# Optimization experiments

Hardware: AMD Instinct MI355X
Metric: run time of the kernel (lower is better)

Reference implementation:

```python
import jax, jax.numpy as jnp
import numpy as np

N_NODES = 100000
N_EDGES = 3200000
IN_CH = 24
HIDDEN = 64
N_CLASSES = 16


def _sage_conv(x, src, dst, W_l, b_l, W_r, num_nodes):
    # mean-aggregate neighbor features at destination nodes
    msg = x[src]                                             # [E, F] gather
    agg = jax.ops.segment_sum(msg, dst, num_segments=num_nodes)
    deg = jax.ops.segment_sum(jnp.ones((src.shape[0],), x.dtype), dst,
                              num_segments=num_nodes)
    mean = agg / jnp.maximum(deg, 1.0)[:, None]
    # PyG SAGEConv: lin_l(aggregated) + lin_r(self); bias lives in lin_l
    return mean @ W_l.T + b_l + x @ W_r.T


def setup_inputs() -> dict:
    key = jax.random.key(0)
    ks = jax.random.split(key, 8)
    x = jax.random.normal(ks[0], (N_NODES, IN_CH), dtype=jnp.float32)
    edge_index = jax.random.randint(ks[1], (2, N_EDGES), 0, N_NODES, dtype=jnp.int64)
    s1 = 1.0 / np.sqrt(IN_CH)
    s2 = 1.0 / np.sqrt(HIDDEN)
    return {
        "x": x,
        "edge_index": edge_index,
        "W1_l": jax.random.normal(ks[2], (HIDDEN, IN_CH), dtype=jnp.float32) * s1,
        "b1": jnp.zeros((HIDDEN,), jnp.float32),
        "W1_r": jax.random.normal(ks[3], (HIDDEN, IN_CH), dtype=jnp.float32) * s1,
        "W2_l": jax.random.normal(ks[4], (HIDDEN, HIDDEN), dtype=jnp.float32) * s2,
        "b2": jnp.zeros((HIDDEN,), jnp.float32),
        "W2_r": jax.random.normal(ks[5], (HIDDEN, HIDDEN), dtype=jnp.float32) * s2,
        "Wc": jax.random.normal(ks[6], (N_CLASSES, HIDDEN), dtype=jnp.float32) * s2,
        "bc": jnp.zeros((N_CLASSES,), jnp.float32),
    }


def reference(x, edge_index, W1_l, b1, W1_r, W2_l, b2, W2_r, Wc, bc):
    num_nodes = x.shape[0]
    src, dst = edge_index[0], edge_index[1]
    h = _sage_conv(x, src, dst, W1_l, b1, W1_r, num_nodes)
    h = jax.nn.relu(h)
    # dropout is identity in eval mode
    embeddings = _sage_conv(h, src, dst, W2_l, b2, W2_r, num_nodes)
    logits = embeddings @ Wc.T + bc
    return (logits, embeddings)
```

## Files before the change

kernel.cpp:

```cpp
#include <hip/hip_runtime.h>

#define N_NODES 100000
#define N_EDGES 3200000
#define IN_CH 24
#define HIDDEN 64
#define N_CLASSES 16

#define NBUCK 782
#define PHBLOCKS 512
#define PHCHUNK 6250
#define PTBLOCKS 256
#define PTCHUNK 12500
#define NSTRIPS (N_NODES / 16)

typedef __attribute__((ext_vector_type(8))) short short8;
typedef __attribute__((ext_vector_type(4))) float float4_;
typedef __attribute__((ext_vector_type(2))) float float2v;

__device__ __forceinline__ unsigned short f2bf(float f) {
    union { float f; unsigned int u; } v; v.f = f;
    unsigned int u = v.u;
    return (unsigned short)((u + 0x7FFFu + ((u >> 16) & 1u)) >> 16);
}
__device__ __forceinline__ unsigned short pk_fp8(float a, float b) {
    return (unsigned short)(__builtin_amdgcn_cvt_pk_fp8_f32(a, b, 0, false) & 0xFFFF);
}
__device__ __forceinline__ void accum8(float2v* A, uint2 u) {
    A[0] += __builtin_amdgcn_cvt_pk_f32_fp8(u.x, false);
    A[1] += __builtin_amdgcn_cvt_pk_f32_fp8(u.x, true);
    A[2] += __builtin_amdgcn_cvt_pk_f32_fp8(u.y, false);
    A[3] += __builtin_amdgcn_cvt_pk_f32_fp8(u.y, true);
}


__global__ __launch_bounds__(1024) void k_phist(const int* __restrict__ dst,
                                                int* __restrict__ bucketCnt) {
    __shared__ int hist[NBUCK];
    int t = threadIdx.x;
    int cbeg = blockIdx.x * PHCHUNK;
    for (int i = t; i < NBUCK; i += 1024) hist[i] = 0;
    __syncthreads();
#pragma unroll
    for (int k = 0; k < 7; k++) {
        int o = k * 1024 + t;
        if (o < PHCHUNK) atomicAdd(&hist[dst[cbeg + o] >> 7], 1);
    }
    __syncthreads();
    for (int i = t; i < NBUCK; i += 1024)
        if (hist[i]) atomicAdd(&bucketCnt[i], hist[i]);
}

__global__ __launch_bounds__(1024) void k_scanb(const int* __restrict__ bucketCnt,
                                                int* __restrict__ bucketBase,
                                                int* __restrict__ bucketFill,
                                                int* __restrict__ srcs, int E) {
    __shared__ int lds[1024];
    int t = threadIdx.x;
    int c = (t < NBUCK) ? bucketCnt[t] : 0;
    int val = c;
    lds[t] = val;
    __syncthreads();
    for (int off = 1; off < 1024; off <<= 1) {
        int v = (t >= off) ? lds[t - off] : 0;
        __syncthreads();
        val += v;
        lds[t] = val;
        __syncthreads();
    }
    if (t < NBUCK) {
        int ex = val - c;
        bucketBase[t] = ex;
        bucketFill[t] = ex;
    }
    if (t == 0) bucketBase[NBUCK] = E;
    if (t < 32) srcs[E + t] = 0;
}

__global__ __launch_bounds__(1024) void k_part(const int* __restrict__ src,
                                               const int* __restrict__ dst,
                                               int* __restrict__ bucketFill,
                                               unsigned int* __restrict__ pedges) {
    __shared__ int cntL[NBUCK];
    __shared__ int baseL[NBUCK];
    int t = threadIdx.x;
    int cbeg = blockIdx.x * PTCHUNK;
    int d[13], s[13];
#pragma unroll
    for (int k = 0; k < 13; k++) {
        int o = k * 1024 + t;
        bool ok = o < PTCHUNK;
        d[k] = ok ? dst[cbeg + o] : -1;
        s[k] = ok ? src[cbeg + o] : 0;
    }
    for (int i = t; i < NBUCK; i += 1024) cntL[i] = 0;
    __syncthreads();
#pragma unroll
    for (int k = 0; k < 13; k++)
        if (d[k] >= 0) atomicAdd(&cntL[d[k] >> 7], 1);
    __syncthreads();
    for (int i = t; i < NBUCK; i += 1024) {
        int c = cntL[i];
        if (c) baseL[i] = atomicAdd(&bucketFill[i], c);
        cntL[i] = 0;
    }
    __syncthreads();
#pragma unroll
    for (int k = 0; k < 13; k++)
        if (d[k] >= 0) {
            int bk = d[k] >> 7;
            int r = atomicAdd(&cntL[bk], 1);
            pedges[baseL[bk] + r] = ((unsigned int)(d[k] & 127) << 17) | (unsigned int)s[k];
        }
}

__global__ __launch_bounds__(1024) void k_bucket(const unsigned int* __restrict__ pedges,
                                                 const int* __restrict__ bucketBase,
                                                 int* __restrict__ rowptr,
                                                 int* __restrict__ srcs, int N, int E) {
    __shared__ int ncnt[128];
    __shared__ int sps[128];
    int b = blockIdx.x;
    int t = threadIdx.x;
    int eb = bucketBase[b], ee = bucketBase[b + 1];
    int m = ee - eb;
    unsigned int v[8];
#pragma unroll
    for (int k = 0; k < 8; k++) {
        int o = k * 1024 + t;
        v[k] = (o < m) ? pedges[eb + o] : 0xFFFFFFFFu;
    }
    if (t < 128) ncnt[t] = 0;
    __syncthreads();
#pragma unroll
    for (int k = 0; k < 8; k++)
        if (v[k] != 0xFFFFFFFFu) atomicAdd(&ncnt[v[k] >> 17], 1);
    __syncthreads();
    int myc = (t < 128) ? ncnt[t] : 0;
    int val = myc;
    if (t < 128) sps[t] = val;
    __syncthreads();
    for (int off = 1; off < 128; off <<= 1) {
        int vv = (t >= off && t < 128) ? sps[t - off] : 0;
        __syncthreads();
        if (t < 128) { val += vv; sps[t] = val; }
        __syncthreads();
    }
    int mybase = val - myc;
    int node = b * 128 + t;
    if (t < 128 && node < N) rowptr[node] = eb + mybase;
    if (b == 0 && t == 0) rowptr[N] = E;
    if (t < 128) { sps[t] = mybase; ncnt[t] = 0; }
    __syncthreads();
#pragma unroll
    for (int k = 0; k < 8; k++)
        if (v[k] != 0xFFFFFFFFu) {
            unsigned int nl = v[k] >> 17;
            int r = atomicAdd(&ncnt[nl], 1);
            srcs[eb + sps[nl] + r] = (int)(v[k] & 0x1FFFF);
        }
}


__global__ __launch_bounds__(256) void k_prep(const float* __restrict__ W1l,
                                              const float* __restrict__ W1r,
                                              const float* __restrict__ W2l,
                                              const float* __restrict__ W2r,
                                              const float* __restrict__ Wc,
                                              const float* __restrict__ b2,
                                              const float* __restrict__ bc,
                                              unsigned short* __restrict__ Bt1,
                                              unsigned short* __restrict__ Bt2,
                                              float* __restrict__ bias2) {
    int t = threadIdx.x;
    for (int i = t; i < 64 * 64; i += 256) {
        int o = i >> 6, k = i & 63;
        float v = (k < 24) ? W1r[o * 24 + k] : ((k < 48) ? W1l[o * 24 + k - 24] : 0.f);
        Bt1[i] = f2bf(v);
    }
    for (int i = t; i < 64 * 128; i += 256) {
        int o = i >> 7, k = i & 127;
        float v = (k < 64) ? W2l[o * 64 + k] : W2r[o * 64 + k - 64];
        Bt2[i] = f2bf(v);
    }
    for (int i = t; i < 16 * 128; i += 256) {
        int c = i >> 7, k = i & 127;
        const float* M = (k < 64) ? W2l : W2r;
        int kk = k & 63;
        float s = 0.f;
        for (int j = 0; j < 64; j++) s += Wc[c * 64 + j] * M[j * 64 + kk];
        Bt2[(64 + c) * 128 + k] = f2bf(s);
    }
    for (int i = t; i < 80; i += 256) {
        if (i < 64) bias2[i] = b2[i];
        else {
            int c = i - 64;
            float s = bc[c];
            for (int j = 0; j < 64; j++) s += Wc[c * 64 + j] * b2[j];
            bias2[i] = s;
        }
    }
}

__global__ __launch_bounds__(256) void k_castx(const float* __restrict__ x,
                                               unsigned int* __restrict__ A1u,
                                               unsigned short* __restrict__ X8s) {
    int gid = blockIdx.x * 256 + threadIdx.x;
    if (gid >= N_NODES * 16) return;
    int n = gid >> 4, kp = gid & 15;
    if (kp < 12) {
        const float2 v = *(const float2*)(x + n * 24 + kp * 2);
        A1u[n * 32 + kp] = (unsigned int)f2bf(v.x) | ((unsigned int)f2bf(v.y) << 16);
        X8s[n * 16 + kp] = pk_fp8(v.x, v.y);
    } else {
        int p = kp - 12;
        uint2 z; z.x = 0u; z.y = 0u;
        *(uint2*)(A1u + n * 32 + 24 + p * 2) = z;
        X8s[n * 16 + kp] = 0;
    }
}


__global__ __launch_bounds__(256) void k_agg1(const unsigned int* __restrict__ X8u,
                                              const int* __restrict__ rowptr,
                                              const int* __restrict__ srcs,
                                              unsigned int* __restrict__ A1w, int N) {
    int node = (blockIdx.x * 256 + threadIdx.x) >> 6;
    int lane = threadIdx.x & 63;
    if (node >= N) return;
    int b = rowptr[node], e = rowptr[node + 1];
    int grp = lane >> 2;
    int sub = lane & 3;
    const unsigned int* basep = X8u + sub * 2;
    float2v A[4] = {{0.f, 0.f}, {0.f, 0.f}, {0.f, 0.f}, {0.f, 0.f}};
    int nfull = (e - b) & ~31;
    int j = b;
    for (; j < b + nfull; j += 32) {
        int s0 = srcs[j + grp];
        int s1 = srcs[j + 16 + grp];
        uint2 u0 = *(const uint2*)(basep + (size_t)s0 * 8);
        uint2 u1 = *(const uint2*)(basep + (size_t)s1 * 8);
        accum8(A, u0);
        accum8(A, u1);
    }
    if (j < e) {
        int j0 = j + grp, j1 = j0 + 16;
        int s0 = srcs[j0], s1 = srcs[j1];
        uint2 u0 = *(const uint2*)(basep + (size_t)s0 * 8);
        uint2 u1 = *(const uint2*)(basep + (size_t)s1 * 8);
        if (j0 >= e) { u0.x = 0; u0.y = 0; }
        if (j1 >= e) { u1.x = 0; u1.y = 0; }
        accum8(A, u0);
        accum8(A, u1);
    }
#pragma unroll
    for (int m = 4; m <= 32; m <<= 1) {
#pragma unroll
        for (int q = 0; q < 4; q++) {
            A[q].x += __shfl_xor(A[q].x, m, 64);
            A[q].y += __shfl_xor(A[q].y, m, 64);
        }
    }
    if (lane < 4) {
        float inv = 1.f / (float)max(e - b, 1);
        uint4 o;
        o.x = (unsigned int)f2bf(A[0].x * inv) | ((unsigned int)f2bf(A[0].y * inv) << 16);
        o.y = (unsigned int)f2bf(A[1].x * inv) | ((unsigned int)f2bf(A[1].y * inv) << 16);
        o.z = (unsigned int)f2bf(A[2].x * inv) | ((unsigned int)f2bf(A[2].y * inv) << 16);
        o.w = (unsigned int)f2bf(A[3].x * inv) | ((unsigned int)f2bf(A[3].y * inv) << 16);
        *(uint4*)(A1w + (size_t)node * 32 + 12 + sub * 4) = o;
    }
}

__global__ __launch_bounds__(256) void k_agg2(const unsigned int* __restrict__ H8u,
                                              const int* __restrict__ rowptr,
                                              const int* __restrict__ srcs,
                                              unsigned int* __restrict__ A2w, int N) {
    int node = (blockIdx.x * 256 + threadIdx.x) >> 6;
    int lane = threadIdx.x & 63;
    if (node >= N) return;
    int b = rowptr[node], e = rowptr[node + 1];
    int grp = lane >> 3;
    int sub = lane & 7;
    const unsigned int* basep = H8u + sub * 2;
    float2v A[4] = {{0.f, 0.f}, {0.f, 0.f}, {0.f, 0.f}, {0.f, 0.f}};
    int nfull = (e - b) & ~31;
    int j = b;
    for (; j < b + nfull; j += 32) {
        int s0 = srcs[j + grp];
        int s1 = srcs[j + 8 + grp];
        int s2 = srcs[j + 16 + grp];
        int s3 = srcs[j + 24 + grp];
        uint2 u0 = *(const uint2*)(basep + (size_t)s0 * 16);
        uint2 u1 = *(const uint2*)(basep + (size_t)s1 * 16);
        uint2 u2 = *(const uint2*)(basep + (size_t)s2 * 16);
        uint2 u3 = *(const uint2*)(basep + (size_t)s3 * 16);
        accum8(A, u0);
        accum8(A, u1);
        accum8(A, u2);
        accum8(A, u3);
    }
    if (j < e) {
        int j0 = j + grp, j1 = j0 + 8, j2 = j0 + 16, j3 = j0 + 24;
        int s0 = srcs[j0], s1 = srcs[j1], s2 = srcs[j2], s3 = srcs[j3];
        uint2 u0 = *(const uint2*)(basep + (size_t)s0 * 16);
        uint2 u1 = *(const uint2*)(basep + (size_t)s1 * 16);
        uint2 u2 = *(const uint2*)(basep + (size_t)s2 * 16);
        uint2 u3 = *(const uint2*)(basep + (size_t)s3 * 16);
        if (j0 >= e) { u0.x = 0; u0.y = 0; }
        if (j1 >= e) { u1.x = 0; u1.y = 0; }
        if (j2 >= e) { u2.x = 0; u2.y = 0; }
        if (j3 >= e) { u3.x = 0; u3.y = 0; }
        accum8(A, u0);
        accum8(A, u1);
        accum8(A, u2);
        accum8(A, u3);
    }
#pragma unroll
    for (int m = 8; m <= 32; m <<= 1) {
#pragma unroll
        for (int q = 0; q < 4; q++) {
            A[q].x += __shfl_xor(A[q].x, m, 64);
            A[q].y += __shfl_xor(A[q].y, m, 64);
        }
    }
    if (lane < 8) {
        float inv = 1.f / (float)max(e - b, 1);
        uint4 o;
        o.x = (unsigned int)f2bf(A[0].x * inv) | ((unsigned int)f2bf(A[0].y * inv) << 16);
        o.y = (unsigned int)f2bf(A[1].x * inv) | ((unsigned int)f2bf(A[1].y * inv) << 16);
        o.z = (unsigned int)f2bf(A[2].x * inv) | ((unsigned int)f2bf(A[2].y * inv) << 16);
        o.w = (unsigned int)f2bf(A[3].x * inv) | ((unsigned int)f2bf(A[3].y * inv) << 16);
        *(uint4*)(A2w + (size_t)node * 64 + sub * 4) = o;
    }
}


__global__ __launch_bounds__(256) void k_gemm1(const unsigned short* __restrict__ A1,
                                               const unsigned short* __restrict__ Bt1,
                                               const float* __restrict__ b1,
                                               unsigned short* __restrict__ A2s,
                                               unsigned char* __restrict__ H8b) {
    int wave = (blockIdx.x * 256 + threadIdx.x) >> 6;
    int lane = threadIdx.x & 63;
    int m = lane & 15, quad = lane >> 4;
    if (wave >= NSTRIPS) return;
    short8 bf[4][2];
#pragma unroll
    for (int t = 0; t < 4; t++)
#pragma unroll
        for (int s = 0; s < 2; s++)
            bf[t][s] = *(const short8*)(Bt1 + (t * 16 + m) * 64 + s * 32 + quad * 8);
    float bias[4];
#pragma unroll
    for (int t = 0; t < 4; t++) bias[t] = b1[t * 16 + m];

    int row0 = wave * 16;
    short8 a0 = *(const short8*)(A1 + (row0 + m) * 64 + quad * 8);
    short8 a1 = *(const short8*)(A1 + (row0 + m) * 64 + 32 + quad * 8);
    float4_ acc[4];
#pragma unroll
    for (int t = 0; t < 4; t++) {
        float4_ c = {0.f, 0.f, 0.f, 0.f};
        c = __builtin_amdgcn_mfma_f32_16x16x32_bf16(a0, bf[t][0], c, 0, 0, 0);
        c = __builtin_amdgcn_mfma_f32_16x16x32_bf16(a1, bf[t][1], c, 0, 0, 0);
        acc[t] = c;
    }
#pragma unroll
    for (int t = 0; t < 4; t++) {
        int col = t * 16 + m;
#pragma unroll
        for (int r = 0; r < 4; r++) {
            int row = row0 + quad * 4 + r;
            float v = fmaxf(acc[t][r] + bias[t], 0.f);
            A2s[row * 128 + 64 + col] = f2bf(v);
            H8b[row * 64 + col] =
                (unsigned char)(__builtin_amdgcn_cvt_pk_fp8_f32(v, 0.f, 0, false) & 0xFF);
        }
    }
}

__global__ __launch_bounds__(256) void k_gemm2(const unsigned short* __restrict__ Bt2,
                                               const float* __restrict__ bias2,
                                               unsigned short* A2s,
                                               float* logits) {
    int wave = (blockIdx.x * 256 + threadIdx.x) >> 6;
    int lane = threadIdx.x & 63;
    int m = lane & 15, quad = lane >> 4;
    if (wave >= NSTRIPS) return;
    short8 bf[5][4];
#pragma unroll
    for (int t = 0; t < 5; t++)
#pragma unroll
        for (int s = 0; s < 4; s++)
            bf[t][s] = *(const short8*)(Bt2 + (t * 16 + m) * 128 + s * 32 + quad * 8);
    float bias[5];
#pragma unroll
    for (int t = 0; t < 5; t++) bias[t] = bias2[t * 16 + m];

    int row0 = wave * 16;
    short8 a[4];
#pragma unroll
    for (int s = 0; s < 4; s++)
        a[s] = *(const short8*)(A2s + (row0 + m) * 128 + s * 32 + quad * 8);
    float4_ acc[5];
#pragma unroll
    for (int t = 0; t < 5; t++) {
        float4_ c = {0.f, 0.f, 0.f, 0.f};
#pragma unroll
        for (int s = 0; s < 4; s++)
            c = __builtin_amdgcn_mfma_f32_16x16x32_bf16(a[s], bf[t][s], c, 0, 0, 0);
        acc[t] = c;
    }
    float* embp = (float*)A2s;
#pragma unroll
    for (int t = 0; t < 4; t++) {
#pragma unroll
        for (int r = 0; r < 4; r++) {
            int row = row0 + quad * 4 + r;
            embp[row * 64 + t * 16 + m] = acc[t][r] + bias[t];
        }
    }
#pragma unroll
    for (int r = 0; r < 4; r++) {
        int row = row0 + quad * 4 + r;
        logits[row * 16 + m] = acc[4][r] + bias[4];
    }
}


extern "C" void kernel_launch(void* const* d_in, const int* in_sizes, int n_in,
                              void* d_out, int out_size, void* d_ws, size_t ws_size,
                              hipStream_t stream) {
    const float* x = (const float*)d_in[0];
    const int* edge = (const int*)d_in[1];
    const int* srcIdx = edge;
    const int* dstIdx = edge + N_EDGES;
    const float* W1l = (const float*)d_in[2];
    const float* b1  = (const float*)d_in[3];
    const float* W1r = (const float*)d_in[4];
    const float* W2l = (const float*)d_in[5];
    const float* b2  = (const float*)d_in[6];
    const float* W2r = (const float*)d_in[7];
    const float* Wc  = (const float*)d_in[8];
    const float* bc  = (const float*)d_in[9];

    float* logits = (float*)d_out;
    unsigned short* A2s = (unsigned short*)((float*)d_out + (size_t)N_NODES * N_CLASSES);
    unsigned int* A2u = (unsigned int*)A2s;

    char* w = (char*)d_ws;
    auto carve = [&](size_t bytes) {
        char* p = w;
        w += (bytes + 255) & ~(size_t)255;
        return p;
    };
    int* rowptr          = (int*)carve((N_NODES + 1) * sizeof(int));
    int* srcs            = (int*)carve((size_t)(N_EDGES + 32) * sizeof(int));
    unsigned int* A1u    = (unsigned int*)carve((size_t)N_NODES * 32 * sizeof(unsigned int));
    unsigned short* X8s  = (unsigned short*)carve((size_t)N_NODES * 32);
    unsigned char* H8b   = (unsigned char*)carve((size_t)N_NODES * 64);
    int* bucketCnt       = (int*)carve(NBUCK * sizeof(int));
    int* bucketBase      = (int*)carve((NBUCK + 1) * sizeof(int));
    int* bucketFill      = (int*)carve(NBUCK * sizeof(int));
    unsigned short* Bt1  = (unsigned short*)carve(64 * 64 * sizeof(unsigned short));
    unsigned short* Bt2  = (unsigned short*)carve(80 * 128 * sizeof(unsigned short));
    float* bias2         = (float*)carve(80 * sizeof(float));

    unsigned int* pedges = (unsigned int*)A1u;
    unsigned short* A1s = (unsigned short*)A1u;
    unsigned int* X8u = (unsigned int*)X8s;
    unsigned int* H8u = (unsigned int*)H8b;

    k_prep<<<1, 256, 0, stream>>>(W1l, W1r, W2l, W2r, Wc, b2, bc, Bt1, Bt2, bias2);

    hipMemsetAsync(bucketCnt, 0, NBUCK * sizeof(int), stream);
    k_phist<<<PHBLOCKS, 1024, 0, stream>>>(dstIdx, bucketCnt);
    k_scanb<<<1, 1024, 0, stream>>>(bucketCnt, bucketBase, bucketFill, srcs, N_EDGES);
    k_part<<<PTBLOCKS, 1024, 0, stream>>>(srcIdx, dstIdx, bucketFill, pedges);
    k_bucket<<<NBUCK, 1024, 0, stream>>>(pedges, bucketBase, rowptr, srcs,
                                         N_NODES, N_EDGES);

    k_castx<<<(N_NODES * 16 + 255) / 256, 256, 0, stream>>>(x, A1u, X8s);
    k_agg1<<<(N_NODES * 64 + 255) / 256, 256, 0, stream>>>(X8u, rowptr, srcs, A1u, N_NODES);
    k_gemm1<<<(NSTRIPS + 3) / 4, 256, 0, stream>>>(A1s, Bt1, b1, A2s, H8b);
    k_agg2<<<(N_NODES * 64 + 255) / 256, 256, 0, stream>>>(H8u, rowptr, srcs, A2u, N_NODES);
    k_gemm2<<<(NSTRIPS + 3) / 4, 256, 0, stream>>>(Bt2, bias2, A2s, logits);
}
```

Measured before the change: 308.9 us.

## Use fixed-capacity buckets to drop histogram pass, split layer-2 aggregation by feature halves

```diff
diff --git a/kernel.cpp b/kernel.cpp
--- a/kernel.cpp
+++ b/kernel.cpp
@@ -7,8 +7,7 @@
 #define N_CLASSES 16
 
 #define NBUCK 782
-#define PHBLOCKS 512
-#define PHCHUNK 6250
+#define CAP 4608
 #define PTBLOCKS 256
 #define PTCHUNK 12500
 #define NSTRIPS (N_NODES / 16)
@@ -33,48 +32,48 @@
 }
 
 
-__global__ __launch_bounds__(1024) void k_phist(const int* __restrict__ dst,
-                                                int* __restrict__ bucketCnt) {
-    __shared__ int hist[NBUCK];
+__global__ __launch_bounds__(256) void k_prep(const float* __restrict__ W1l,
+                                              const float* __restrict__ W1r,
+                                              const float* __restrict__ W2l,
+                                              const float* __restrict__ W2r,
+                                              const float* __restrict__ Wc,
+                                              const float* __restrict__ b2,
+                                              const float* __restrict__ bc,
+                                              unsigned short* __restrict__ Bt1,
+                                              unsigned short* __restrict__ Bt2,
+                                              float* __restrict__ bias2,
+                                              int* __restrict__ bucketFill) {
     int t = threadIdx.x;
-    int cbeg = blockIdx.x * PHCHUNK;
-    for (int i = t; i < NBUCK; i += 1024) hist[i] = 0;
-    __syncthreads();
-#pragma unroll
-    for (int k = 0; k < 7; k++) {
-        int o = k * 1024 + t;
-        if (o < PHCHUNK) atomicAdd(&hist[dst[cbeg + o] >> 7], 1);
-    }
-    __syncthreads();
-    for (int i = t; i < NBUCK; i += 1024)
-        if (hist[i]) atomicAdd(&bucketCnt[i], hist[i]);
-}
-
-__global__ __launch_bounds__(1024) void k_scanb(const int* __restrict__ bucketCnt,
-                                                int* __restrict__ bucketBase,
-                                                int* __restrict__ bucketFill,
-                                                int* __restrict__ srcs, int E) {
-    __shared__ int lds[1024];
-    int t = threadIdx.x;
-    int c = (t < NBUCK) ? bucketCnt[t] : 0;
-    int val = c;
-    lds[t] = val;
-    __syncthreads();
-    for (int off = 1; off < 1024; off <<= 1) {
-        int v = (t >= off) ? lds[t - off] : 0;
-        __syncthreads();
-        val += v;
-        lds[t] = val;
-        __syncthreads();
-    }
-    if (t < NBUCK) {
-        int ex = val - c;
-        bucketBase[t] = ex;
-        bucketFill[t] = ex;
-    }
-    if (t == 0) bucketBase[NBUCK] = E;
-    if (t < 32) srcs[E + t] = 0;
-}
+    for (int i = t; i < NBUCK; i += 256) bucketFill[i] = 0;
+    for (int i = t; i < 64 * 64; i += 256) {
+        int o = i >> 6, k = i & 63;
+        float v = (k < 24) ? W1r[o * 24 + k] : ((k < 48) ? W1l[o * 24 + k - 24] : 0.f);
+        Bt1[i] = f2bf(v);
+    }
+    for (int i = t; i < 64 * 128; i += 256) {
+        int o = i >> 7, k = i & 127;
+        float v = (k < 64) ? W2l[o * 64 + k] : W2r[o * 64 + k - 64];
+        Bt2[i] = f2bf(v);
+    }
+    for (int i = t; i < 16 * 128; i += 256) {
+        int c = i >> 7, k = i & 127;
+        const float* M = (k < 64) ? W2l : W2r;
+        int kk = k & 63;
+        float s = 0.f;
+        for (int j = 0; j < 64; j++) s += Wc[c * 64 + j] * M[j * 64 + kk];
+        Bt2[(64 + c) * 128 + k] = f2bf(s);
+    }
+    for (int i = t; i < 80; i += 256) {
+        if (i < 64) bias2[i] = b2[i];
+        else {
+            int c = i - 64;
+            float s = bc[c];
+            for (int j = 0; j < 64; j++) s += Wc[c * 64 + j] * b2[j];
+            bias2[i] = s;
+        }
+    }
+}
+
 
 __global__ __launch_bounds__(1024) void k_part(const int* __restrict__ src,
                                                const int* __restrict__ dst,
@@ -100,7 +99,7 @@
     __syncthreads();
     for (int i = t; i < NBUCK; i += 1024) {
         int c = cntL[i];
-        if (c) baseL[i] = atomicAdd(&bucketFill[i], c);
+        if (c) baseL[i] = i * CAP + atomicAdd(&bucketFill[i], c);
         cntL[i] = 0;
     }
     __syncthreads();
@@ -114,25 +113,25 @@
 }
 
 __global__ __launch_bounds__(1024) void k_bucket(const unsigned int* __restrict__ pedges,
-                                                 const int* __restrict__ bucketBase,
-                                                 int* __restrict__ rowptr,
-                                                 int* __restrict__ srcs, int N, int E) {
+                                                 const int* __restrict__ bucketFill,
+                                                 int2* __restrict__ begend,
+                                                 int* __restrict__ srcs, int N) {
     __shared__ int ncnt[128];
     __shared__ int sps[128];
     int b = blockIdx.x;
     int t = threadIdx.x;
-    int eb = bucketBase[b], ee = bucketBase[b + 1];
-    int m = ee - eb;
-    unsigned int v[8];
-#pragma unroll
-    for (int k = 0; k < 8; k++) {
+    int eb0 = b * CAP;
+    int m = bucketFill[b];
+    unsigned int v[5];
+#pragma unroll
+    for (int k = 0; k < 5; k++) {
         int o = k * 1024 + t;
-        v[k] = (o < m) ? pedges[eb + o] : 0xFFFFFFFFu;
+        v[k] = (o < m) ? pedges[eb0 + o] : 0xFFFFFFFFu;
     }
     if (t < 128) ncnt[t] = 0;
     __syncthreads();
 #pragma unroll
-    for (int k = 0; k < 8; k++)
+    for (int k = 0; k < 5; k++)
         if (v[k] != 0xFFFFFFFFu) atomicAdd(&ncnt[v[k] >> 17], 1);
     __syncthreads();
     int myc = (t < 128) ? ncnt[t] : 0;
@@ -147,58 +146,20 @@
     }
     int mybase = val - myc;
     int node = b * 128 + t;
-    if (t < 128 && node < N) rowptr[node] = eb + mybase;
-    if (b == 0 && t == 0) rowptr[N] = E;
+    if (t < 128 && node < N) {
+        int2 be; be.x = eb0 + mybase; be.y = eb0 + mybase + myc;
+        begend[node] = be;
+    }
     if (t < 128) { sps[t] = mybase; ncnt[t] = 0; }
-    __syncthreads();
-#pragma unroll
-    for (int k = 0; k < 8; k++)
+    if (t < 32) srcs[eb0 + m + t] = 0;
+    __syncthreads();
+#pragma unroll
+    for (int k = 0; k < 5; k++)
         if (v[k] != 0xFFFFFFFFu) {
             unsigned int nl = v[k] >> 17;
             int r = atomicAdd(&ncnt[nl], 1);
-            srcs[eb + sps[nl] + r] = (int)(v[k] & 0x1FFFF);
-        }
-}
-
-
-__global__ __launch_bounds__(256) void k_prep(const float* __restrict__ W1l,
-                                              const float* __restrict__ W1r,
-                                              const float* __restrict__ W2l,
-                                              const float* __restrict__ W2r,
-                                              const float* __restrict__ Wc,
-                                              const float* __restrict__ b2,
-                                              const float* __restrict__ bc,
-                                              unsigned short* __restrict__ Bt1,
-                                              unsigned short* __restrict__ Bt2,
-                                              float* __restrict__ bias2) {
-    int t = threadIdx.x;
-    for (int i = t; i < 64 * 64; i += 256) {
-        int o = i >> 6, k = i & 63;
-        float v = (k < 24) ? W1r[o * 24 + k] : ((k < 48) ? W1l[o * 24 + k - 24] : 0.f);
-        Bt1[i] = f2bf(v);
-    }
-    for (int i = t; i < 64 * 128; i += 256) {
-        int o = i >> 7, k = i & 127;
-        float v = (k < 64) ? W2l[o * 64 + k] : W2r[o * 64 + k - 64];
-        Bt2[i] = f2bf(v);
-    }
-    for (int i = t; i < 16 * 128; i += 256) {
-        int c = i >> 7, k = i & 127;
-        const float* M = (k < 64) ? W2l : W2r;
-        int kk = k & 63;
-        float s = 0.f;
-        for (int j = 0; j < 64; j++) s += Wc[c * 64 + j] * M[j * 64 + kk];
-        Bt2[(64 + c) * 128 + k] = f2bf(s);
-    }
-    for (int i = t; i < 80; i += 256) {
-        if (i < 64) bias2[i] = b2[i];
-        else {
-            int c = i - 64;
-            float s = bc[c];
-            for (int j = 0; j < 64; j++) s += Wc[c * 64 + j] * b2[j];
-            bias2[i] = s;
-        }
-    }
+            srcs[eb0 + sps[nl] + r] = (int)(v[k] & 0x1FFFF);
+        }
 }
 
 __global__ __launch_bounds__(256) void k_castx(const float* __restrict__ x,
@@ -221,13 +182,14 @@
 
 
 __global__ __launch_bounds__(256) void k_agg1(const unsigned int* __restrict__ X8u,
-                                              const int* __restrict__ rowptr,
+                                              const int2* __restrict__ begend,
                                               const int* __restrict__ srcs,
                                               unsigned int* __restrict__ A1w, int N) {
     int node = (blockIdx.x * 256 + threadIdx.x) >> 6;
     int lane = threadIdx.x & 63;
     if (node >= N) return;
-    int b = rowptr[node], e = rowptr[node + 1];
+    int2 be = begend[node];
+    int b = be.x, e = be.y;
     int grp = lane >> 2;
     int sub = lane & 3;
     const unsigned int* basep = X8u + sub * 2;
@@ -271,66 +233,56 @@
     }
 }
 
-__global__ __launch_bounds__(256) void k_agg2(const unsigned int* __restrict__ H8u,
-                                              const int* __restrict__ rowptr,
-                                              const int* __restrict__ srcs,
-                                              unsigned int* __restrict__ A2w, int N) {
+__global__ __launch_bounds__(256) void k_agg2s(const unsigned int* __restrict__ T8u,
+                                               const int2* __restrict__ begend,
+                                               const int* __restrict__ srcs,
+                                               unsigned int* __restrict__ A2w,
+                                               int outOff, int N) {
     int node = (blockIdx.x * 256 + threadIdx.x) >> 6;
     int lane = threadIdx.x & 63;
     if (node >= N) return;
-    int b = rowptr[node], e = rowptr[node + 1];
-    int grp = lane >> 3;
-    int sub = lane & 7;
-    const unsigned int* basep = H8u + sub * 2;
+    int2 be = begend[node];
+    int b = be.x, e = be.y;
+    int grp = lane >> 2;
+    int sub = lane & 3;
+    const unsigned int* basep = T8u + sub * 2;
     float2v A[4] = {{0.f, 0.f}, {0.f, 0.f}, {0.f, 0.f}, {0.f, 0.f}};
     int nfull = (e - b) & ~31;
     int j = b;
     for (; j < b + nfull; j += 32) {
         int s0 = srcs[j + grp];
-        int s1 = srcs[j + 8 + grp];
-        int s2 = srcs[j + 16 + grp];
-        int s3 = srcs[j + 24 + grp];
-        uint2 u0 = *(const uint2*)(basep + (size_t)s0 * 16);
-        uint2 u1 = *(const uint2*)(basep + (size_t)s1 * 16);
-        uint2 u2 = *(const uint2*)(basep + (size_t)s2 * 16);
-        uint2 u3 = *(const uint2*)(basep + (size_t)s3 * 16);
+        int s1 = srcs[j + 16 + grp];
+        uint2 u0 = *(const uint2*)(basep + (size_t)s0 * 8);
+        uint2 u1 = *(const uint2*)(basep + (size_t)s1 * 8);
         accum8(A, u0);
         accum8(A, u1);
-        accum8(A, u2);
-        accum8(A, u3);
     }
     if (j < e) {
-        int j0 = j + grp, j1 = j0 + 8, j2 = j0 + 16, j3 = j0 + 24;
-        int s0 = srcs[j0], s1 = srcs[j1], s2 = srcs[j2], s3 = srcs[j3];
-        uint2 u0 = *(const uint2*)(basep + (size_t)s0 * 16);
-        uint2 u1 = *(const uint2*)(basep + (size_t)s1 * 16);
-        uint2 u2 = *(const uint2*)(basep + (size_t)s2 * 16);
-        uint2 u3 = *(const uint2*)(basep + (size_t)s3 * 16);
+        int j0 = j + grp, j1 = j0 + 16;
+        int s0 = srcs[j0], s1 = srcs[j1];
+        uint2 u0 = *(const uint2*)(basep + (size_t)s0 * 8);
+        uint2 u1 = *(const uint2*)(basep + (size_t)s1 * 8);
         if (j0 >= e) { u0.x = 0; u0.y = 0; }
         if (j1 >= e) { u1.x = 0; u1.y = 0; }
-        if (j2 >= e) { u2.x = 0; u2.y = 0; }
-        if (j3 >= e) { u3.x = 0; u3.y = 0; }
         accum8(A, u0);
         accum8(A, u1);
-        accum8(A, u2);
-        accum8(A, u3);
-    }
-#pragma unroll
-    for (int m = 8; m <= 32; m <<= 1) {
+    }
+#pragma unroll
+    for (int m = 4; m <= 32; m <<= 1) {
 #pragma unroll
         for (int q = 0; q < 4; q++) {
             A[q].x += __shfl_xor(A[q].x, m, 64);
             A[q].y += __shfl_xor(A[q].y, m, 64);
         }
     }
-    if (lane < 8) {
+    if (lane < 4) {
         float inv = 1.f / (float)max(e - b, 1);
         uint4 o;
         o.x = (unsigned int)f2bf(A[0].x * inv) | ((unsigned int)f2bf(A[0].y * inv) << 16);
         o.y = (unsigned int)f2bf(A[1].x * inv) | ((unsigned int)f2bf(A[1].y * inv) << 16);
         o.z = (unsigned int)f2bf(A[2].x * inv) | ((unsigned int)f2bf(A[2].y * inv) << 16);
         o.w = (unsigned int)f2bf(A[3].x * inv) | ((unsigned int)f2bf(A[3].y * inv) << 16);
-        *(uint4*)(A2w + (size_t)node * 64 + sub * 4) = o;
+        *(uint4*)(A2w + (size_t)node * 64 + outOff + sub * 4) = o;
     }
 }
 
@@ -339,6 +291,7 @@
                                                const unsigned short* __restrict__ Bt1,
                                                const float* __restrict__ b1,
                                                unsigned short* __restrict__ A2s,
+                                               unsigned char* __restrict__ H8a,
                                                unsigned char* __restrict__ H8b) {
     int wave = (blockIdx.x * 256 + threadIdx.x) >> 6;
     int lane = threadIdx.x & 63;
@@ -368,12 +321,14 @@
 #pragma unroll
     for (int t = 0; t < 4; t++) {
         int col = t * 16 + m;
+        unsigned char* H8 = (t < 2) ? H8a : H8b;
+        int hcol = (t < 2) ? col : col - 32;
 #pragma unroll
         for (int r = 0; r < 4; r++) {
             int row = row0 + quad * 4 + r;
             float v = fmaxf(acc[t][r] + bias[t], 0.f);
             A2s[row * 128 + 64 + col] = f2bf(v);
-            H8b[row * 64 + col] =
+            H8[row * 32 + hcol] =
                 (unsigned char)(__builtin_amdgcn_cvt_pk_fp8_f32(v, 0.f, 0, false) & 0xFF);
         }
     }
@@ -454,13 +409,12 @@
         w += (bytes + 255) & ~(size_t)255;
         return p;
     };
-    int* rowptr          = (int*)carve((N_NODES + 1) * sizeof(int));
-    int* srcs            = (int*)carve((size_t)(N_EDGES + 32) * sizeof(int));
+    int2* begend         = (int2*)carve((size_t)N_NODES * sizeof(int2));
+    int* srcs            = (int*)carve((size_t)NBUCK * CAP * sizeof(int));
     unsigned int* A1u    = (unsigned int*)carve((size_t)N_NODES * 32 * sizeof(unsigned int));
     unsigned short* X8s  = (unsigned short*)carve((size_t)N_NODES * 32);
-    unsigned char* H8b   = (unsigned char*)carve((size_t)N_NODES * 64);
-    int* bucketCnt       = (int*)carve(NBUCK * sizeof(int));
-    int* bucketBase      = (int*)carve((NBUCK + 1) * sizeof(int));
+    unsigned char* H8a   = (unsigned char*)carve((size_t)N_NODES * 32);
+    unsigned char* H8b   = (unsigned char*)carve((size_t)N_NODES * 32);
     int* bucketFill      = (int*)carve(NBUCK * sizeof(int));
     unsigned short* Bt1  = (unsigned short*)carve(64 * 64 * sizeof(unsigned short));
     unsigned short* Bt2  = (unsigned short*)carve(80 * 128 * sizeof(unsigned short));
@@ -469,20 +423,19 @@
     unsigned int* pedges = (unsigned int*)A1u;
     unsigned short* A1s = (unsigned short*)A1u;
     unsigned int* X8u = (unsigned int*)X8s;
-    unsigned int* H8u = (unsigned int*)H8b;
-
-    k_prep<<<1, 256, 0, stream>>>(W1l, W1r, W2l, W2r, Wc, b2, bc, Bt1, Bt2, bias2);
-
-    hipMemsetAsync(bucketCnt, 0, NBUCK * sizeof(int), stream);
-    k_phist<<<PHBLOCKS, 1024, 0, stream>>>(dstIdx, bucketCnt);
-    k_scanb<<<1, 1024, 0, stream>>>(bucketCnt, bucketBase, bucketFill, srcs, N_EDGES);
+    unsigned int* H8au = (unsigned int*)H8a;
+    unsigned int* H8bu = (unsigned int*)H8b;
+
+    k_prep<<<1, 256, 0, stream>>>(W1l, W1r, W2l, W2r, Wc, b2, bc, Bt1, Bt2, bias2,
+                                  bucketFill);
     k_part<<<PTBLOCKS, 1024, 0, stream>>>(srcIdx, dstIdx, bucketFill, pedges);
-    k_bucket<<<NBUCK, 1024, 0, stream>>>(pedges, bucketBase, rowptr, srcs,
-                                         N_NODES, N_EDGES);
+    k_bucket<<<NBUCK, 1024, 0, stream>>>(pedges, bucketFill, begend, srcs, N_NODES);
 
     k_castx<<<(N_NODES * 16 + 255) / 256, 256, 0, stream>>>(x, A1u, X8s);
-    k_agg1<<<(N_NODES * 64 + 255) / 256, 256, 0, stream>>>(X8u, rowptr, srcs, A1u, N_NODES);
-    k_gemm1<<<(NSTRIPS + 3) / 4, 256, 0, stream>>>(A1s, Bt1, b1, A2s, H8b);
-    k_agg2<<<(N_NODES * 64 + 255) / 256, 256, 0, stream>>>(H8u, rowptr, srcs, A2u, N_NODES);
+    int agrid = (N_NODES * 64 + 255) / 256;
+    k_agg1<<<agrid, 256, 0, stream>>>(X8u, begend, srcs, A1u, N_NODES);
+    k_gemm1<<<(NSTRIPS + 3) / 4, 256, 0, stream>>>(A1s, Bt1, b1, A2s, H8a, H8b);
+    k_agg2s<<<agrid, 256, 0, stream>>>(H8au, begend, srcs, A2u, 0, N_NODES);
+    k_agg2s<<<agrid, 256, 0, stream>>>(H8bu, begend, srcs, A2u, 16, N_NODES);
     k_gemm2<<<(NSTRIPS + 3) / 4, 256, 0, stream>>>(Bt2, bias2, A2s, logits);
 }
```

Result: slower. 316.9 us (+2.6%).
